# Performance work log

Measured on AMD Instinct MI355X. Metric: run time of the kernel, lower is better.

Reference implementation:

```python
import jax, jax.numpy as jnp
import numpy as np

DIM = 768
NUM_HEADS = 12
HEAD_DIM = DIM // NUM_HEADS


def setup_inputs() -> dict:
    key = jax.random.key(0)
    k1, k2, k3 = jax.random.split(key, 3)
    B, N, C = 1, 4096, DIM
    x = jax.random.normal(k1, (B, N, C), dtype=jnp.float32)
    w_qkv = jax.random.normal(k2, (C, 3 * C), dtype=jnp.float32) * (C ** -0.5)
    w_proj = jax.random.normal(k3, (C, C), dtype=jnp.float32) * (C ** -0.5)
    b_proj = jnp.zeros((C,), dtype=jnp.float32)
    return {"x": x, "w_qkv": w_qkv, "w_proj": w_proj, "b_proj": b_proj}


def reference(x, w_qkv, w_proj, b_proj):
    B, N, C = x.shape
    H, D = NUM_HEADS, HEAD_DIM
    scale = D ** -0.5
    # QKV projection (no bias), split into heads: [B, N, 3, H, D] -> bhnd
    qkv = (x @ w_qkv).reshape(B, N, 3, H, D)
    qkv = jnp.transpose(qkv, (2, 0, 3, 1, 4))  # [3, B, H, N, D]
    q, k, v = qkv[0], qkv[1], qkv[2]
    # world_size == 1 => all_gather is identity; full attention over N
    attn = jnp.einsum('bhnd,bhmd->bhnm', q * scale, k)
    attn = jax.nn.softmax(attn, axis=-1)
    out = jnp.einsum('bhnm,bhmd->bhnd', attn, v)
    out = jnp.transpose(out, (0, 2, 1, 3)).reshape(B, N, C)
    return out @ w_proj + b_proj
```

## Files before the change

kernel.cpp:

```cpp
#include <hip/hip_runtime.h>
#include <hip/hip_bf16.h>

#define NT 4096
#define CD 768
#define NH 12
#define HD 64
#define CQ 2304

typedef __bf16 bf;
typedef __bf16 v8bf __attribute__((ext_vector_type(8)));
typedef __bf16 v4bf __attribute__((ext_vector_type(4)));
typedef float  v4f  __attribute__((ext_vector_type(4)));

__device__ __forceinline__ void gld16(const bf* g, bf* l) {
  __builtin_amdgcn_global_load_lds(
      (__attribute__((address_space(1))) void*)g,
      (__attribute__((address_space(3))) void*)l,
      16, 0, 0);
}

__device__ __forceinline__ float fexp2(float x) {
#if defined(__HIP_DEVICE_COMPILE__)
  return __builtin_amdgcn_exp2f(x);
#else
  return x;
#endif
}

__global__ __launch_bounds__(256) void prep(
    const float* __restrict__ x, const float* __restrict__ wqkv,
    const float* __restrict__ wproj, bf* __restrict__ Xb,
    bf* __restrict__ WqkvT, bf* __restrict__ WpT) {
  __shared__ float tile[32][33];
  const int b = blockIdx.x, tid = threadIdx.x;
  if (b < 3072) {
    const int i = b * 256 + tid;
    const float4 v = ((const float4*)x)[i];
    bf o4[4] = {(bf)v.x, (bf)v.y, (bf)v.z, (bf)v.w};
    ((ushort4*)Xb)[i] = *(const ushort4*)o4;
    return;
  }
  const float* in;
  bf* out;
  int rows, cols, c0, r0;
  if (b < 4800) {
    const int t = b - 3072;
    in = wqkv; out = WqkvT; rows = CD; cols = CQ;
    c0 = (t % 72) * 32; r0 = (t / 72) * 32;
  } else {
    const int t = b - 4800;
    in = wproj; out = WpT; rows = CD; cols = CD;
    c0 = (t % 24) * 32; r0 = (t / 24) * 32;
  }
  const int tx = tid & 31, ty = tid >> 5;
#pragma unroll
  for (int j = 0; j < 32; j += 8)
    tile[ty + j][tx] = in[(size_t)(r0 + ty + j) * cols + (c0 + tx)];
  __syncthreads();
#pragma unroll
  for (int j = 0; j < 32; j += 8)
    out[(size_t)(c0 + ty + j) * rows + (r0 + tx)] = (bf)tile[tx][ty + j];
}

__global__ __launch_bounds__(256, 3) void gemm_qkv(
    const bf* __restrict__ A, const bf* __restrict__ Bt,
    bf* __restrict__ Qb, bf* __restrict__ Kb, bf* __restrict__ Vtb) {
  __shared__ __align__(16) bf As[128 * 64];
  __shared__ __align__(16) bf Bs[128 * 64];
  const int tid = threadIdx.x;
  const int lane = tid & 63, wave = tid >> 6;
  const int lane15 = lane & 15, quad = lane >> 4;
  const int waveM = wave & 1, waveN = wave >> 1;
  const int bm = blockIdx.x * 128;
  const int bn = blockIdx.y * 128;

  v4f acc[4][4];
#pragma unroll
  for (int i = 0; i < 4; ++i)
#pragma unroll
    for (int j = 0; j < 4; ++j) acc[i][j] = (v4f){0.f, 0.f, 0.f, 0.f};

  for (int k0 = 0; k0 < CD; k0 += 64) {
#pragma unroll
    for (int p = 0; p < 4; ++p) {
      const int t = tid + p * 256;
      const int r = t >> 3, u = t & 7;
      gld16(A + (size_t)(bm + r) * CD + k0 + ((u ^ (r & 7)) << 3), As + t * 8);
    }
#pragma unroll
    for (int p = 0; p < 4; ++p) {
      const int t = tid + p * 256;
      const int r = t >> 3, u = t & 7;
      gld16(Bt + (size_t)(bn + r) * CD + k0 + ((u ^ (r & 7)) << 3), Bs + t * 8);
    }
    asm volatile("s_waitcnt vmcnt(0)" ::: "memory");
    __syncthreads();

    v8bf af[4][2], bfr[4][2];
#pragma unroll
    for (int mt = 0; mt < 4; ++mt) {
      const int rr = waveM * 64 + mt * 16 + lane15;
      const int r7 = rr & 7;
      af[mt][0] = *(const v8bf*)(As + rr * 64 + ((quad ^ r7) << 3));
      af[mt][1] = *(const v8bf*)(As + rr * 64 + (((quad ^ 4) ^ r7) << 3));
    }
#pragma unroll
    for (int nt = 0; nt < 4; ++nt) {
      const int rr = waveN * 64 + nt * 16 + lane15;
      const int r7 = rr & 7;
      bfr[nt][0] = *(const v8bf*)(Bs + rr * 64 + ((quad ^ r7) << 3));
      bfr[nt][1] = *(const v8bf*)(Bs + rr * 64 + (((quad ^ 4) ^ r7) << 3));
    }
#pragma unroll
    for (int mt = 0; mt < 4; ++mt)
#pragma unroll
      for (int nt = 0; nt < 4; ++nt) {
        acc[mt][nt] = __builtin_amdgcn_mfma_f32_16x16x32_bf16(af[mt][0], bfr[nt][0], acc[mt][nt], 0, 0, 0);
        acc[mt][nt] = __builtin_amdgcn_mfma_f32_16x16x32_bf16(af[mt][1], bfr[nt][1], acc[mt][nt], 0, 0, 0);
      }
    __syncthreads();
  }

  const float QSCALE = 0.125f * 1.4426950408889634f;
#pragma unroll
  for (int mt = 0; mt < 4; ++mt) {
    const int rowB = bm + waveM * 64 + mt * 16 + quad * 4;
#pragma unroll
    for (int nt = 0; nt < 4; ++nt) {
      const int col = bn + waveN * 64 + nt * 16 + lane15;
      const int s = col / CD;
      const int rem = col - s * CD;
      const int h = rem >> 6, d = rem & 63;
      if (s == 2) {
        bf vp[4];
#pragma unroll
        for (int i = 0; i < 4; ++i) vp[i] = (bf)acc[mt][nt][i];
        const int pos = (rowB & ~31) + (((rowB & 15) >> 2) << 3) + (((rowB >> 4) & 1) << 2);
        *(uint2*)(Vtb + ((size_t)h * HD + d) * NT + pos) = *(const uint2*)vp;
      } else {
#pragma unroll
        for (int i = 0; i < 4; ++i) {
          const float v = acc[mt][nt][i];
          const int row = rowB + i;
          if (s == 0) Qb[((size_t)h * NT + row) * HD + d] = (bf)(v * QSCALE);
          else        Kb[((size_t)h * NT + row) * HD + d] = (bf)v;
        }
      }
    }
  }
}

__global__ __launch_bounds__(256, 2) void attn(
    const bf* __restrict__ Qb, const bf* __restrict__ Kb,
    const bf* __restrict__ Vtb, bf* __restrict__ Ob) {
  __shared__ __align__(16) char smem[65536];
  float* Red = (float*)smem;

  const int b = blockIdx.x;
  int h, qt;
  if (b < 512) { h = b & 7;        qt = b >> 3; }
  else { const int bb = b - 512; h = 8 + (bb & 3); qt = bb >> 2; }
  const int q0 = qt * 64;

  const int tid = threadIdx.x;
  const int wave = tid >> 6, lane = tid & 63;
  const int lane15 = lane & 15, quad = lane >> 4;

  const bf* Kh = Kb + (size_t)h * NT * HD;
  const bf* Vh = Vtb + (size_t)h * HD * NT;

  v8bf aQ[4][2];
#pragma unroll
  for (int sub = 0; sub < 4; ++sub) {
    const int qrow = q0 + sub * 16 + lane15;
    aQ[sub][0] = *(const v8bf*)(Qb + ((size_t)h * NT + qrow) * HD + quad * 8);
    aQ[sub][1] = *(const v8bf*)(Qb + ((size_t)h * NT + qrow) * HD + 32 + quad * 8);
  }

  v4f o[4][4];
#pragma unroll
  for (int sub = 0; sub < 4; ++sub)
#pragma unroll
    for (int dt = 0; dt < 4; ++dt) o[sub][dt] = (v4f){0.f, 0.f, 0.f, 0.f};
  float lsum[4] = {0.f, 0.f, 0.f, 0.f};

  auto stage = [&](int half, int kt) {
    bf* Kdst = (bf*)(smem + half * 32768);
    bf* Vdst = (bf*)(smem + half * 32768 + 16384);
#pragma unroll
    for (int p = 0; p < 4; ++p) {
      const int L = p * 256 + tid;
      const int r = L >> 3, u = L & 7;
      gld16(Kh + (size_t)(kt + r) * HD + ((u ^ (r & 7)) << 3), Kdst + L * 8);
    }
#pragma unroll
    for (int p = 0; p < 4; ++p) {
      const int L = p * 256 + tid;
      const int d = L >> 4, u = L & 15;
      gld16(Vh + (size_t)d * NT + kt + ((u ^ (d & 15)) << 3), Vdst + L * 8);
    }
  };

  stage(0, 0);
  asm volatile("s_waitcnt vmcnt(0)" ::: "memory");
  __syncthreads();

  for (int it = 0; it < NT / 128; ++it) {
    const int half = it & 1;
    if (it + 1 < NT / 128) stage(half ^ 1, (it + 1) * 128);

    const bf* Kbuf = (const bf*)(smem + half * 32768);
    const bf* Vbuf = (const bf*)(smem + half * 32768 + 16384);

    v4bf aPlo[4], aPhi[4];
#pragma unroll
    for (int e = 0; e < 2; ++e) {
      const int k = (wave * 2 + e) * 16 + lane15;
      const int k7 = k & 7;
      const v8bf bk0 = *(const v8bf*)(Kbuf + k * 64 + ((quad ^ k7) << 3));
      const v8bf bk1 = *(const v8bf*)(Kbuf + k * 64 + (((quad ^ 4) ^ k7) << 3));
#pragma unroll
      for (int sub = 0; sub < 4; ++sub) {
        v4f z = (v4f){0.f, 0.f, 0.f, 0.f};
        z = __builtin_amdgcn_mfma_f32_16x16x32_bf16(bk0, aQ[sub][0], z, 0, 0, 0);
        z = __builtin_amdgcn_mfma_f32_16x16x32_bf16(bk1, aQ[sub][1], z, 0, 0, 0);
        v4bf p4;
#pragma unroll
        for (int r = 0; r < 4; ++r) {
          const float p = fexp2(z[r]);
          lsum[sub] += p;
          p4[r] = (bf)p;
        }
        if (e == 0) aPlo[sub] = p4; else aPhi[sub] = p4;
      }
    }

#pragma unroll
    for (int dt = 0; dt < 4; ++dt) {
      const int d = dt * 16 + lane15;
      const v8bf bv = *(const v8bf*)(Vbuf + d * 128 + (((wave * 4 + quad) ^ lane15) << 3));
#pragma unroll
      for (int sub = 0; sub < 4; ++sub) {
        const v8bf aP8 = __builtin_shufflevector(aPlo[sub], aPhi[sub], 0, 1, 2, 3, 4, 5, 6, 7);
        o[sub][dt] = __builtin_amdgcn_mfma_f32_16x16x32_bf16(aP8, bv, o[sub][dt], 0, 0, 0);
      }
    }

    asm volatile("s_waitcnt vmcnt(0)" ::: "memory");
    __syncthreads();
  }

#pragma unroll
  for (int sub = 0; sub < 4; ++sub) {
    lsum[sub] += __shfl_xor(lsum[sub], 16, 64);
    lsum[sub] += __shfl_xor(lsum[sub], 32, 64);
  }

#pragma unroll
  for (int sp = 0; sp < 2; ++sp) {
    __syncthreads();
#pragma unroll
    for (int sl = 0; sl < 2; ++sl) {
      const int s = sp * 2 + sl;
      float* reg = Red + (wave * 2 + sl) * 1024;
#pragma unroll
      for (int dt = 0; dt < 4; ++dt)
        *(v4f*)(reg + dt * 256 + lane15 * 16 + quad * 4) = o[s][dt];
      if (quad == 0) Red[8192 + (wave * 2 + sl) * 16 + lane15] = lsum[s];
    }
    __syncthreads();
    const int wlo = sp * 2;
    if (wave == wlo || wave == wlo + 1) {
      const int sl = wave - wlo;
      const int s = sp * 2 + sl;
      float den = 0.f;
#pragma unroll
      for (int wv = 0; wv < 4; ++wv) den += Red[8192 + (wv * 2 + sl) * 16 + lane15];
      const float linv = 1.f / den;
#pragma unroll
      for (int dt = 0; dt < 4; ++dt) {
        v4f sum = (v4f){0.f, 0.f, 0.f, 0.f};
#pragma unroll
        for (int wv = 0; wv < 4; ++wv)
          sum += *(const v4f*)(Red + (wv * 2 + sl) * 1024 + dt * 256 + lane15 * 16 + quad * 4);
#pragma unroll
        for (int i = 0; i < 4; ++i) {
          const float linv_i = __shfl(linv, quad * 4 + i, 64);
          const int row = q0 + s * 16 + quad * 4 + i;
          Ob[(size_t)row * CD + h * HD + dt * 16 + lane15] = (bf)(sum[i] * linv_i);
        }
      }
    }
  }
}

__global__ __launch_bounds__(256, 4) void gemm_proj(
    const bf* __restrict__ A, const bf* __restrict__ Bt,
    const float* __restrict__ bias, float* __restrict__ out) {
  __shared__ __align__(16) bf As[2][64 * 32];
  __shared__ __align__(16) bf Bs[2][128 * 32];
  const int tid = threadIdx.x;
  const int lane = tid & 63, wave = tid >> 6;
  const int lane15 = lane & 15, quad = lane >> 4;
  const int bm = blockIdx.x * 64;
  const int bn = blockIdx.y * 128;

  v4f acc[4][2];
#pragma unroll
  for (int i = 0; i < 4; ++i)
#pragma unroll
    for (int j = 0; j < 2; ++j) acc[i][j] = (v4f){0.f, 0.f, 0.f, 0.f};

  auto stageG = [&](int half, int k0) {
    {
      const int r = tid >> 2, c = (tid & 3) * 8;
      gld16(A + (size_t)(bm + r) * CD + k0 + c, As[half] + tid * 8);
    }
#pragma unroll
    for (int p = 0; p < 2; ++p) {
      const int t = tid + p * 256;
      const int r = t >> 2, c = (t & 3) * 8;
      gld16(Bt + (size_t)(bn + r) * CD + k0 + c, Bs[half] + t * 8);
    }
  };

  stageG(0, 0);
  asm volatile("s_waitcnt vmcnt(0)" ::: "memory");
  __syncthreads();

  for (int it = 0; it < CD / 32; ++it) {
    const int half = it & 1;
    if (it + 1 < CD / 32) stageG(half ^ 1, (it + 1) * 32);

    v8bf af[4], bfr[2];
#pragma unroll
    for (int mt = 0; mt < 4; ++mt)
      af[mt] = *(const v8bf*)(As[half] + (mt * 16 + lane15) * 32 + quad * 8);
#pragma unroll
    for (int nt = 0; nt < 2; ++nt)
      bfr[nt] = *(const v8bf*)(Bs[half] + (wave * 32 + nt * 16 + lane15) * 32 + quad * 8);
#pragma unroll
    for (int mt = 0; mt < 4; ++mt)
#pragma unroll
      for (int nt = 0; nt < 2; ++nt)
        acc[mt][nt] = __builtin_amdgcn_mfma_f32_16x16x32_bf16(af[mt], bfr[nt], acc[mt][nt], 0, 0, 0);

    asm volatile("s_waitcnt vmcnt(0)" ::: "memory");
    __syncthreads();
  }

#pragma unroll
  for (int mt = 0; mt < 4; ++mt) {
    const int rowB = bm + mt * 16 + quad * 4;
#pragma unroll
    for (int nt = 0; nt < 2; ++nt) {
      const int col = bn + wave * 32 + nt * 16 + lane15;
      const float bcol = bias[col];
#pragma unroll
      for (int i = 0; i < 4; ++i)
        out[(size_t)(rowB + i) * CD + col] = acc[mt][nt][i] + bcol;
    }
  }
}

extern "C" void kernel_launch(void* const* d_in, const int* in_sizes, int n_in,
                              void* d_out, int out_size, void* d_ws, size_t ws_size,
                              hipStream_t stream) {
  const float* x     = (const float*)d_in[0];
  const float* wqkv  = (const float*)d_in[1];
  const float* wproj = (const float*)d_in[2];
  const float* bproj = (const float*)d_in[3];
  float* out = (float*)d_out;

  bf* ws    = (bf*)d_ws;
  bf* Xb    = ws;  ws += (size_t)NT * CD;
  bf* WqkvT = ws;  ws += (size_t)CQ * CD;
  bf* WpT   = ws;  ws += (size_t)CD * CD;
  bf* Qb    = ws;  ws += (size_t)NH * NT * HD;
  bf* Kb    = ws;  ws += (size_t)NH * NT * HD;
  bf* Vtb   = ws;  ws += (size_t)NH * NT * HD;
  bf* Ob    = ws;  ws += (size_t)NT * CD;

  prep<<<5376, 256, 0, stream>>>(x, wqkv, wproj, Xb, WqkvT, WpT);
  gemm_qkv<<<dim3(NT / 128, CQ / 128), 256, 0, stream>>>(Xb, WqkvT, Qb, Kb, Vtb);
  attn<<<768, 256, 0, stream>>>(Qb, Kb, Vtb, Ob);
  gemm_proj<<<dim3(NT / 64, CD / 128), 256, 0, stream>>>(Ob, WpT, bproj, out);
}
```

Before: 171.1 us.

## Split attention waves 2x2 over query/key, halve LDS tile, raise occupancy

Reorganises the attention kernel so the four waves form a 2x2 grid: each wave owns two of the four 16-row query slices and half of each key tile. The key/value tile shrinks from 128 to 64 keys, halving LDS to 32 KB, and launch bounds rise from 2 to 4 blocks per CU to hide latency. MFMA sections are wrapped in s_setprio. The final cross-wave reduction now combines only two partials per slice. The cost is twice as many loop iterations and barriers, plus more K/V reloads across blocks.

```diff
diff --git a/kernel.cpp b/kernel.cpp
--- a/kernel.cpp
+++ b/kernel.cpp
@@ -150,11 +150,10 @@
   }
 }
 
-__global__ __launch_bounds__(256, 2) void attn(
+__global__ __launch_bounds__(256, 4) void attn(
     const bf* __restrict__ Qb, const bf* __restrict__ Kb,
     const bf* __restrict__ Vtb, bf* __restrict__ Ob) {
-  __shared__ __align__(16) char smem[65536];
-  float* Red = (float*)smem;
+  __shared__ __align__(16) char smem[32768];
 
   const int b = blockIdx.x;
   int h, qt;
@@ -164,40 +163,42 @@
 
   const int tid = threadIdx.x;
   const int wave = tid >> 6, lane = tid & 63;
+  const int kh = wave & 1;
+  const int sh = wave >> 1;
   const int lane15 = lane & 15, quad = lane >> 4;
 
   const bf* Kh = Kb + (size_t)h * NT * HD;
   const bf* Vh = Vtb + (size_t)h * HD * NT;
 
-  v8bf aQ[4][2];
-#pragma unroll
-  for (int sub = 0; sub < 4; ++sub) {
-    const int qrow = q0 + sub * 16 + lane15;
-    aQ[sub][0] = *(const v8bf*)(Qb + ((size_t)h * NT + qrow) * HD + quad * 8);
-    aQ[sub][1] = *(const v8bf*)(Qb + ((size_t)h * NT + qrow) * HD + 32 + quad * 8);
-  }
-
-  v4f o[4][4];
-#pragma unroll
-  for (int sub = 0; sub < 4; ++sub)
-#pragma unroll
-    for (int dt = 0; dt < 4; ++dt) o[sub][dt] = (v4f){0.f, 0.f, 0.f, 0.f};
-  float lsum[4] = {0.f, 0.f, 0.f, 0.f};
+  v8bf aQ[2][2];
+#pragma unroll
+  for (int sl = 0; sl < 2; ++sl) {
+    const int qrow = q0 + (sh * 2 + sl) * 16 + lane15;
+    aQ[sl][0] = *(const v8bf*)(Qb + ((size_t)h * NT + qrow) * HD + quad * 8);
+    aQ[sl][1] = *(const v8bf*)(Qb + ((size_t)h * NT + qrow) * HD + 32 + quad * 8);
+  }
+
+  v4f o[2][4];
+#pragma unroll
+  for (int sl = 0; sl < 2; ++sl)
+#pragma unroll
+    for (int dt = 0; dt < 4; ++dt) o[sl][dt] = (v4f){0.f, 0.f, 0.f, 0.f};
+  float lsum[2] = {0.f, 0.f};
 
   auto stage = [&](int half, int kt) {
-    bf* Kdst = (bf*)(smem + half * 32768);
-    bf* Vdst = (bf*)(smem + half * 32768 + 16384);
-#pragma unroll
-    for (int p = 0; p < 4; ++p) {
+    bf* Kdst = (bf*)(smem + half * 16384);
+    bf* Vdst = (bf*)(smem + half * 16384 + 8192);
+#pragma unroll
+    for (int p = 0; p < 2; ++p) {
       const int L = p * 256 + tid;
       const int r = L >> 3, u = L & 7;
       gld16(Kh + (size_t)(kt + r) * HD + ((u ^ (r & 7)) << 3), Kdst + L * 8);
     }
 #pragma unroll
-    for (int p = 0; p < 4; ++p) {
+    for (int p = 0; p < 2; ++p) {
       const int L = p * 256 + tid;
-      const int d = L >> 4, u = L & 15;
-      gld16(Vh + (size_t)d * NT + kt + ((u ^ (d & 15)) << 3), Vdst + L * 8);
+      const int d = L >> 3, u = L & 7;
+      gld16(Vh + (size_t)d * NT + kt + ((u ^ (d & 7)) << 3), Vdst + L * 8);
     }
   };
 
@@ -205,45 +206,49 @@
   asm volatile("s_waitcnt vmcnt(0)" ::: "memory");
   __syncthreads();
 
-  for (int it = 0; it < NT / 128; ++it) {
+  for (int it = 0; it < NT / 64; ++it) {
     const int half = it & 1;
-    if (it + 1 < NT / 128) stage(half ^ 1, (it + 1) * 128);
-
-    const bf* Kbuf = (const bf*)(smem + half * 32768);
-    const bf* Vbuf = (const bf*)(smem + half * 32768 + 16384);
-
-    v4bf aPlo[4], aPhi[4];
+    if (it + 1 < NT / 64) stage(half ^ 1, (it + 1) * 64);
+
+    const bf* Kbuf = (const bf*)(smem + half * 16384);
+    const bf* Vbuf = (const bf*)(smem + half * 16384 + 8192);
+
+    v4bf aPlo[2], aPhi[2];
 #pragma unroll
     for (int e = 0; e < 2; ++e) {
-      const int k = (wave * 2 + e) * 16 + lane15;
+      const int k = kh * 32 + e * 16 + lane15;
       const int k7 = k & 7;
       const v8bf bk0 = *(const v8bf*)(Kbuf + k * 64 + ((quad ^ k7) << 3));
       const v8bf bk1 = *(const v8bf*)(Kbuf + k * 64 + (((quad ^ 4) ^ k7) << 3));
 #pragma unroll
-      for (int sub = 0; sub < 4; ++sub) {
+      for (int sl = 0; sl < 2; ++sl) {
         v4f z = (v4f){0.f, 0.f, 0.f, 0.f};
-        z = __builtin_amdgcn_mfma_f32_16x16x32_bf16(bk0, aQ[sub][0], z, 0, 0, 0);
-        z = __builtin_amdgcn_mfma_f32_16x16x32_bf16(bk1, aQ[sub][1], z, 0, 0, 0);
+        __builtin_amdgcn_s_setprio(1);
+        z = __builtin_amdgcn_mfma_f32_16x16x32_bf16(bk0, aQ[sl][0], z, 0, 0, 0);
+        z = __builtin_amdgcn_mfma_f32_16x16x32_bf16(bk1, aQ[sl][1], z, 0, 0, 0);
+        __builtin_amdgcn_s_setprio(0);
         v4bf p4;
 #pragma unroll
         for (int r = 0; r < 4; ++r) {
           const float p = fexp2(z[r]);
-          lsum[sub] += p;
+          lsum[sl] += p;
           p4[r] = (bf)p;
         }
-        if (e == 0) aPlo[sub] = p4; else aPhi[sub] = p4;
+        if (e == 0) aPlo[sl] = p4; else aPhi[sl] = p4;
       }
     }
 
 #pragma unroll
     for (int dt = 0; dt < 4; ++dt) {
       const int d = dt * 16 + lane15;
-      const v8bf bv = *(const v8bf*)(Vbuf + d * 128 + (((wave * 4 + quad) ^ lane15) << 3));
-#pragma unroll
-      for (int sub = 0; sub < 4; ++sub) {
-        const v8bf aP8 = __builtin_shufflevector(aPlo[sub], aPhi[sub], 0, 1, 2, 3, 4, 5, 6, 7);
-        o[sub][dt] = __builtin_amdgcn_mfma_f32_16x16x32_bf16(aP8, bv, o[sub][dt], 0, 0, 0);
-      }
+      const v8bf bv = *(const v8bf*)(Vbuf + d * 64 + (((kh * 4 + quad) ^ (d & 7)) << 3));
+      __builtin_amdgcn_s_setprio(1);
+#pragma unroll
+      for (int sl = 0; sl < 2; ++sl) {
+        const v8bf aP8 = __builtin_shufflevector(aPlo[sl], aPhi[sl], 0, 1, 2, 3, 4, 5, 6, 7);
+        o[sl][dt] = __builtin_amdgcn_mfma_f32_16x16x32_bf16(aP8, bv, o[sl][dt], 0, 0, 0);
+      }
+      __builtin_amdgcn_s_setprio(0);
     }
 
     asm volatile("s_waitcnt vmcnt(0)" ::: "memory");
@@ -251,44 +256,35 @@
   }
 
 #pragma unroll
-  for (int sub = 0; sub < 4; ++sub) {
-    lsum[sub] += __shfl_xor(lsum[sub], 16, 64);
-    lsum[sub] += __shfl_xor(lsum[sub], 32, 64);
-  }
-
-#pragma unroll
-  for (int sp = 0; sp < 2; ++sp) {
-    __syncthreads();
-#pragma unroll
-    for (int sl = 0; sl < 2; ++sl) {
-      const int s = sp * 2 + sl;
-      float* reg = Red + (wave * 2 + sl) * 1024;
-#pragma unroll
-      for (int dt = 0; dt < 4; ++dt)
-        *(v4f*)(reg + dt * 256 + lane15 * 16 + quad * 4) = o[s][dt];
-      if (quad == 0) Red[8192 + (wave * 2 + sl) * 16 + lane15] = lsum[s];
-    }
-    __syncthreads();
-    const int wlo = sp * 2;
-    if (wave == wlo || wave == wlo + 1) {
-      const int sl = wave - wlo;
-      const int s = sp * 2 + sl;
-      float den = 0.f;
-#pragma unroll
-      for (int wv = 0; wv < 4; ++wv) den += Red[8192 + (wv * 2 + sl) * 16 + lane15];
-      const float linv = 1.f / den;
-#pragma unroll
-      for (int dt = 0; dt < 4; ++dt) {
-        v4f sum = (v4f){0.f, 0.f, 0.f, 0.f};
-#pragma unroll
-        for (int wv = 0; wv < 4; ++wv)
-          sum += *(const v4f*)(Red + (wv * 2 + sl) * 1024 + dt * 256 + lane15 * 16 + quad * 4);
-#pragma unroll
-        for (int i = 0; i < 4; ++i) {
-          const float linv_i = __shfl(linv, quad * 4 + i, 64);
-          const int row = q0 + s * 16 + quad * 4 + i;
-          Ob[(size_t)row * CD + h * HD + dt * 16 + lane15] = (bf)(sum[i] * linv_i);
-        }
+  for (int sl = 0; sl < 2; ++sl) {
+    lsum[sl] += __shfl_xor(lsum[sl], 16, 64);
+    lsum[sl] += __shfl_xor(lsum[sl], 32, 64);
+  }
+
+  float* Red = (float*)smem;
+  float* Ls  = (float*)(smem + 16384);
+#pragma unroll
+  for (int sl = 0; sl < 2; ++sl) {
+    __syncthreads();
+    float* reg = Red + wave * 1024;
+#pragma unroll
+    for (int dt = 0; dt < 4; ++dt)
+      *(v4f*)(reg + dt * 256 + lane15 * 16 + quad * 4) = o[sl][dt];
+    if (quad == 0) Ls[wave * 16 + lane15] = lsum[sl];
+    __syncthreads();
+    const int s = sh * 2 + sl;
+    const float den = Ls[(sh * 2) * 16 + lane15] + Ls[(sh * 2 + 1) * 16 + lane15];
+    const float linv = 1.f / den;
+#pragma unroll
+    for (int dh = 0; dh < 2; ++dh) {
+      const int dt = kh * 2 + dh;
+      v4f sum = *(const v4f*)(Red + (sh * 2) * 1024 + dt * 256 + lane15 * 16 + quad * 4);
+      sum     += *(const v4f*)(Red + (sh * 2 + 1) * 1024 + dt * 256 + lane15 * 16 + quad * 4);
+#pragma unroll
+      for (int i = 0; i < 4; ++i) {
+        const float linv_i = __shfl(linv, quad * 4 + i, 64);
+        const int row = q0 + s * 16 + quad * 4 + i;
+        Ob[(size_t)row * CD + h * HD + dt * 16 + lane15] = (bf)(sum[i] * linv_i);
       }
     }
   }
```

New measurement: 171.0 us. About the same (-0.0%).
